# Performance work log

Measured on AMD Instinct MI355X. Metric: run time of the kernel, lower is better.

Reference implementation:

```python
import jax, jax.numpy as jnp
import numpy as np

B, T, I, H, L, C = 64, 512, 128, 512, 3, 5


def setup_inputs() -> dict:
    key = jax.random.key(0)
    ks = jax.random.split(key, 2 + 4 * L + 2)
    s = 1.0 / np.sqrt(H)  # PyTorch RNN init range
    inp = {"x": jax.random.normal(ks[0], (B, T, I), dtype=jnp.float32)}
    in_dims = [I] + [H] * (L - 1)
    for l in range(L):
        k0, k1, k2, k3 = ks[1 + 4 * l:5 + 4 * l]
        inp[f"W_ih{l}"] = jax.random.uniform(k0, (H, in_dims[l]), jnp.float32, -s, s)
        inp[f"W_hh{l}"] = jax.random.uniform(k1, (H, H), jnp.float32, -s, s)
        inp[f"b_ih{l}"] = jax.random.uniform(k2, (H,), jnp.float32, -s, s)
        inp[f"b_hh{l}"] = jax.random.uniform(k3, (H,), jnp.float32, -s, s)
    so = 1.0 / np.sqrt(H)
    inp["W_out"] = jax.random.uniform(ks[-2], (C, H), jnp.float32, -so, so)
    inp["b_out"] = jax.random.uniform(ks[-1], (C,), jnp.float32, -so, so)
    return inp


def _rnn_layer(xs, W_ih, W_hh, b_ih, b_hh):
    # xs: [B, T, D] -> hidden sequence [B, T, H], ReLU RNN recurrence
    h0 = jnp.zeros((xs.shape[0], W_hh.shape[0]), xs.dtype)
    xproj = jnp.einsum('btd,hd->bth', xs, W_ih) + (b_ih + b_hh)  # precompute input GEMM

    def step(h, xp_t):
        h = jax.nn.relu(xp_t + h @ W_hh.T)
        return h, h

    _, ys = jax.lax.scan(step, h0, jnp.swapaxes(xproj, 0, 1))  # scan over time
    return jnp.swapaxes(ys, 0, 1)


def reference(x, W_ih0, W_hh0, b_ih0, b_hh0, W_ih1, W_hh1, b_ih1, b_hh1,
              W_ih2, W_hh2, b_ih2, b_hh2, W_out, b_out):
    h = x
    for W_ih, W_hh, b_ih, b_hh in ((W_ih0, W_hh0, b_ih0, b_hh0),
                                   (W_ih1, W_hh1, b_ih1, b_hh1),
                                   (W_ih2, W_hh2, b_ih2, b_hh2)):
        h = _rnn_layer(h, W_ih, W_hh, b_ih, b_hh)
    # last timestep -> linear head: [B, C]
    return h[:, -1, :] @ W_out.T + b_out
```

## Files before the change

kernel.cpp:

```cpp
#include <hip/hip_runtime.h>

#define BB 64
#define TT 512
#define II 128
#define HH 512
#define CC 5

__global__ __launch_bounds__(256) void gemm_bias_kernel(
    const float* __restrict__ A, const float* __restrict__ W,
    const float* __restrict__ b1, const float* __restrict__ b2,
    float* __restrict__ out, int K)
{
    __shared__ float As[16][132];
    __shared__ float Bs[16][132];
    const int tid = threadIdx.x;
    const int bm = blockIdx.x;
    const int bn = blockIdx.y;
    const int tx = tid & 15;
    const int ty = tid >> 4;
    const int lr = tid >> 2;
    const int lk = (tid & 3) << 2;

    const float* Ab = A + (size_t)bm * 128 * K;
    const float* Wb = W + (size_t)bn * 128 * K;

    float acc[8][8];
#pragma unroll
    for (int i = 0; i < 8; ++i)
#pragma unroll
        for (int j = 0; j < 8; ++j) acc[i][j] = 0.f;

    for (int k0 = 0; k0 < K; k0 += 16) {
        float4 a0 = *(const float4*)(Ab + (size_t)lr * K + k0 + lk);
        float4 a1 = *(const float4*)(Ab + (size_t)(lr + 64) * K + k0 + lk);
        float4 w0 = *(const float4*)(Wb + (size_t)lr * K + k0 + lk);
        float4 w1 = *(const float4*)(Wb + (size_t)(lr + 64) * K + k0 + lk);
        __syncthreads();
        As[lk + 0][lr] = a0.x; As[lk + 1][lr] = a0.y; As[lk + 2][lr] = a0.z; As[lk + 3][lr] = a0.w;
        As[lk + 0][lr + 64] = a1.x; As[lk + 1][lr + 64] = a1.y; As[lk + 2][lr + 64] = a1.z; As[lk + 3][lr + 64] = a1.w;
        Bs[lk + 0][lr] = w0.x; Bs[lk + 1][lr] = w0.y; Bs[lk + 2][lr] = w0.z; Bs[lk + 3][lr] = w0.w;
        Bs[lk + 0][lr + 64] = w1.x; Bs[lk + 1][lr + 64] = w1.y; Bs[lk + 2][lr + 64] = w1.z; Bs[lk + 3][lr + 64] = w1.w;
        __syncthreads();
#pragma unroll
        for (int k = 0; k < 16; ++k) {
            float4 av0 = *(const float4*)&As[k][ty * 8];
            float4 av1 = *(const float4*)&As[k][ty * 8 + 4];
            float4 bv0 = *(const float4*)&Bs[k][tx * 8];
            float4 bv1 = *(const float4*)&Bs[k][tx * 8 + 4];
            float a[8] = {av0.x, av0.y, av0.z, av0.w, av1.x, av1.y, av1.z, av1.w};
            float b[8] = {bv0.x, bv0.y, bv0.z, bv0.w, bv1.x, bv1.y, bv1.z, bv1.w};
#pragma unroll
            for (int i = 0; i < 8; ++i)
#pragma unroll
                for (int j = 0; j < 8; ++j)
                    acc[i][j] = fmaf(a[i], b[j], acc[i][j]);
        }
    }

    const int nb = bn * 128 + tx * 8;
    float bias[8];
#pragma unroll
    for (int j = 0; j < 8; ++j) bias[j] = b1[nb + j] + b2[nb + j];
#pragma unroll
    for (int i = 0; i < 8; ++i) {
        const size_t m = (size_t)bm * 128 + ty * 8 + i;
        float4 o0 = {acc[i][0] + bias[0], acc[i][1] + bias[1], acc[i][2] + bias[2], acc[i][3] + bias[3]};
        float4 o1 = {acc[i][4] + bias[4], acc[i][5] + bias[5], acc[i][6] + bias[6], acc[i][7] + bias[7]};
        *(float4*)(out + m * HH + nb) = o0;
        *(float4*)(out + m * HH + nb + 4) = o1;
    }
}

__global__ __launch_bounds__(512)
__attribute__((amdgpu_waves_per_eu(2, 2)))
void scan_kernel(
    const float* __restrict__ xp, const float* __restrict__ Whh,
    float* __restrict__ y, unsigned long long* hbuf)
{
    __shared__ float hbs[4][2][8 * 68];
    __shared__ int written[8];

    const int tid  = threadIdx.x;
    const int s    = blockIdx.x >> 5;
    const int g    = blockIdx.x & 31;
    const int lane = tid & 63;
    const int wv   = tid >> 6;
    const int rloc = lane >> 3;
    const int kseg = lane & 7;
    const int R    = s * 64 + wv * 8 + rloc;

    const float* wr = Whh + (size_t)R * HH + kseg * 64;
    const float4 w0  = *(const float4*)(wr + 0);
    const float4 w1  = *(const float4*)(wr + 4);
    const float4 w2  = *(const float4*)(wr + 8);
    const float4 w3  = *(const float4*)(wr + 12);
    const float4 w4  = *(const float4*)(wr + 16);
    const float4 w5  = *(const float4*)(wr + 20);
    const float4 w6  = *(const float4*)(wr + 24);
    const float4 w7  = *(const float4*)(wr + 28);
    const float4 w8  = *(const float4*)(wr + 32);
    const float4 w9  = *(const float4*)(wr + 36);
    const float4 w10 = *(const float4*)(wr + 40);
    const float4 w11 = *(const float4*)(wr + 44);
    const float4 w12 = *(const float4*)(wr + 48);
    const float4 w13 = *(const float4*)(wr + 52);
    const float4 w14 = *(const float4*)(wr + 56);
    const float4 w15 = *(const float4*)(wr + 60);

    unsigned long long* gbase = hbuf + (size_t)g * 2048;
    const int gb0 = g * 2, gb1 = g * 2 + 1;

    const int lds_w    = wv * 68 + lane;
    const int self_lds = s * 68 + wv * 8 + rloc;
    const bool pub     = (kseg == 0);
    const bool foreign = (wv != s);

    hbs[0][0][lds_w] = 0.f;
    hbs[0][1][lds_w] = 0.f;
    if (tid < 8) written[tid] = 0;

    float xp0 = 0.f, xp1 = 0.f;
    if (pub) {
        xp0 = xp[(size_t)gb0 * TT * HH + R];
        xp1 = xp[(size_t)gb1 * TT * HH + R];
    }
    __syncthreads();

    for (int t = 0; t < TT; ++t) {
        if (t > 0) {
            for (;;) {
                int m = __hip_atomic_load(&written[0], __ATOMIC_RELAXED,
                                          __HIP_MEMORY_SCOPE_WORKGROUP);
#pragma unroll
                for (int c = 1; c < 8; ++c) {
                    int wc = __hip_atomic_load(&written[c], __ATOMIC_RELAXED,
                                               __HIP_MEMORY_SCOPE_WORKGROUP);
                    m = (wc < m) ? wc : m;
                }
                if (m >= t) break;
            }
            __threadfence_block();
        }

        const int bi = t & 3;
        float a0 = 0.f, a1 = 0.f, c0 = 0.f, c1 = 0.f;
        const float* h0p = &hbs[bi][0][kseg * 68];
        const float* h1p = &hbs[bi][1][kseg * 68];
#define STEP4(WQ, OFF)                                                   \
        {                                                                \
            float4 h0 = *(const float4*)(h0p + (OFF));                   \
            float4 h1 = *(const float4*)(h1p + (OFF));                   \
            a0 = fmaf(WQ.x, h0.x, a0); a1 = fmaf(WQ.y, h0.y, a1);        \
            a0 = fmaf(WQ.z, h0.z, a0); a1 = fmaf(WQ.w, h0.w, a1);        \
            c0 = fmaf(WQ.x, h1.x, c0); c1 = fmaf(WQ.y, h1.y, c1);        \
            c0 = fmaf(WQ.z, h1.z, c0); c1 = fmaf(WQ.w, h1.w, c1);        \
        }
        STEP4(w0, 0)   STEP4(w1, 4)   STEP4(w2, 8)   STEP4(w3, 12)
        STEP4(w4, 16)  STEP4(w5, 20)  STEP4(w6, 24)  STEP4(w7, 28)
        STEP4(w8, 32)  STEP4(w9, 36)  STEP4(w10, 40) STEP4(w11, 44)
        STEP4(w12, 48) STEP4(w13, 52) STEP4(w14, 56) STEP4(w15, 60)
#undef STEP4

        float A = a0 + a1, Bv = c0 + c1;
        A  += __shfl_xor(A, 1);  A  += __shfl_xor(A, 2);  A  += __shfl_xor(A, 4);
        Bv += __shfl_xor(Bv, 1); Bv += __shfl_xor(Bv, 2); Bv += __shfl_xor(Bv, 4);

        const int q = t + 1;
        unsigned long long* slotp = gbase + (q & 3) * 512;
        const unsigned int phase = 1u ^ (((unsigned)(q - 1) >> 2) & 1u);

        float hn0 = 0.f, hn1 = 0.f;
        if (pub) {
            hn0 = fmaxf(A + xp0, 0.f);
            hn1 = fmaxf(Bv + xp1, 0.f);
            if (q < TT) {
                const unsigned long long pkt =
                    (unsigned long long)(__float_as_uint(hn0) | (phase << 31)) |
                    ((unsigned long long)(__float_as_uint(hn1) | (phase << 31)) << 32);
                __hip_atomic_store(slotp + R, pkt,
                                   __ATOMIC_RELAXED, __HIP_MEMORY_SCOPE_AGENT);
                hbs[q & 3][0][self_lds] = hn0;
                hbs[q & 3][1][self_lds] = hn1;
            }
            y[((size_t)gb0 * TT + t) * HH + R] = hn0;
            y[((size_t)gb1 * TT + t) * HH + R] = hn1;
            if (q < TT) {
                xp0 = xp[((size_t)gb0 * TT + q) * HH + R];
                xp1 = xp[((size_t)gb1 * TT + q) * HH + R];
            }
        }

        if (q < TT) {
            if (foreign) {
                unsigned long long u;
                for (;;) {
                    u = __hip_atomic_load(slotp + tid, __ATOMIC_RELAXED,
                                          __HIP_MEMORY_SCOPE_AGENT);
                    if ((((unsigned int)(u >> 31) & 1u) == phase) &&
                        ((unsigned int)(u >> 63) == phase)) break;
                }
                hbs[q & 3][0][lds_w] = __uint_as_float((unsigned int)u & 0x7fffffffu);
                hbs[q & 3][1][lds_w] = __uint_as_float((unsigned int)(u >> 32) & 0x7fffffffu);
            }
            __threadfence_block();
            if (lane == 0)
                __hip_atomic_store(&written[wv], q, __ATOMIC_RELAXED,
                                   __HIP_MEMORY_SCOPE_WORKGROUP);
        }
    }
}

__global__ __launch_bounds__(64) void head_kernel(
    const float* __restrict__ y2, const float* __restrict__ Wout,
    const float* __restrict__ bout, float* __restrict__ out)
{
    const int bc = blockIdx.x;
    const int b = bc / CC, c = bc % CC;
    const int lane = threadIdx.x;
    const float* yrow = y2 + ((size_t)b * TT + (TT - 1)) * HH;
    const float* wrow = Wout + (size_t)c * HH;
    float s = 0.f;
#pragma unroll
    for (int i = 0; i < HH / 64; ++i)
        s = fmaf(yrow[lane + 64 * i], wrow[lane + 64 * i], s);
#pragma unroll
    for (int off = 32; off > 0; off >>= 1) s += __shfl_down(s, off);
    if (lane == 0) out[bc] = s + bout[c];
}

extern "C" void kernel_launch(void* const* d_in, const int* in_sizes, int n_in,
                              void* d_out, int out_size, void* d_ws, size_t ws_size,
                              hipStream_t stream)
{
    const float* x = (const float*)d_in[0];
    const float* W_ih[3] = {(const float*)d_in[1], (const float*)d_in[5], (const float*)d_in[9]};
    const float* W_hh[3] = {(const float*)d_in[2], (const float*)d_in[6], (const float*)d_in[10]};
    const float* b_ih[3] = {(const float*)d_in[3], (const float*)d_in[7], (const float*)d_in[11]};
    const float* b_hh[3] = {(const float*)d_in[4], (const float*)d_in[8], (const float*)d_in[12]};
    const float* W_out = (const float*)d_in[13];
    const float* b_out = (const float*)d_in[14];
    float* out = (float*)d_out;

    float* ws   = (float*)d_ws;
    float* Y    = ws;
    float* XP   = ws + (size_t)BB * TT * HH;
    unsigned long long* hbuf = (unsigned long long*)(XP + (size_t)BB * TT * HH);

    const size_t hbuf_bytes = 32 * 4 * 512 * sizeof(unsigned long long);
    const dim3 ggrid(256, 4, 1);

    gemm_bias_kernel<<<ggrid, 256, 0, stream>>>(x, W_ih[0], b_ih[0], b_hh[0], XP, II);
    (void)hipMemsetAsync(hbuf, 0, hbuf_bytes, stream);
    scan_kernel<<<256, 512, 0, stream>>>(XP, W_hh[0], Y, hbuf);
    gemm_bias_kernel<<<ggrid, 256, 0, stream>>>(Y, W_ih[1], b_ih[1], b_hh[1], XP, HH);
    (void)hipMemsetAsync(hbuf, 0, hbuf_bytes, stream);
    scan_kernel<<<256, 512, 0, stream>>>(XP, W_hh[1], Y, hbuf);
    gemm_bias_kernel<<<ggrid, 256, 0, stream>>>(Y, W_ih[2], b_ih[2], b_hh[2], XP, HH);
    (void)hipMemsetAsync(hbuf, 0, hbuf_bytes, stream);
    scan_kernel<<<256, 512, 0, stream>>>(XP, W_hh[2], Y, hbuf);
    head_kernel<<<BB * CC, 64, 0, stream>>>(Y, W_out, b_out, out);
}
```

Baseline: 2.673 ms.

## Pipeline layer 0 and layer 1 scans concurrently with fused input projection

Replaces the per-layer GEMM + scan sequence with a wavefront pipeline. Layer-0 scan blocks and fused layer-1 blocks run in one launch. Layer 1 consumes layer-0 outputs per timestep through flagged global packets and computes the input projection inline alongside the recurrence, and layer 2 runs as a separate fused kernel. This removes two GEMM launches and the serialization between layer scans. In exchange it adds large memsets of full-history flag buffers, more global polling traffic, and relies on all 512 co-resident blocks making forward progress.

New measurement: 4.267 ms. 1.6x slower.

```diff
diff --git a/kernel.cpp b/kernel.cpp
--- a/kernel.cpp
+++ b/kernel.cpp
@@ -5,6 +5,43 @@
 #define II 128
 #define HH 512
 #define CC 5
+
+
+#define FPAD(v) ((((v) >> 5) * 36) + ((v) & 31))
+#define M31LO(u) __uint_as_float((unsigned int)(u) & 0x7fffffffu)
+#define M31HI(u) __uint_as_float((unsigned int)((u) >> 32) & 0x7fffffffu)
+
+struct FSh {
+    float hbs[2][4][16 * 36];
+    float ybs[2][4][16 * 36];
+    int written[8];
+};
+struct SSh {
+    float hbs[4][2][8 * 68];
+    int written[8];
+};
+union ShU { FSh f; SSh s; };
+
+__device__ __forceinline__ bool prdy(unsigned long long u, int set) {
+    const unsigned int hi = (unsigned int)(u >> 63) & 1u;
+    const unsigned int lo = (unsigned int)(u >> 31) & 1u;
+    return set ? (hi && lo) : (hi && !lo);
+}
+
+template <int M>
+__device__ __forceinline__ const unsigned long long* src_addr(
+    const unsigned long long* mainb, const unsigned long long* sideb,
+    int gp, int t, int v, int half)
+{
+    if constexpr (M == 2) {
+        return mainb + (((size_t)(2 * gp + half) * 512 + t) * 512 + v);
+    } else if constexpr (M == 0) {
+        if (t >= 2) return mainb + (((size_t)(2 * gp + half) * 512 + (t - 2)) * 512 + v);
+        return sideb + (((size_t)(gp * 2 + t) * 512 + v) * 2 + half);
+    } else {
+        return mainb + (((size_t)gp * 512 + t) * 512 + v) * 2 + half;
+    }
+}
 
 __global__ __launch_bounds__(256) void gemm_bias_kernel(
     const float* __restrict__ A, const float* __restrict__ W,
@@ -71,18 +108,12 @@
     }
 }
 
-__global__ __launch_bounds__(512)
-__attribute__((amdgpu_waves_per_eu(2, 2)))
-void scan_kernel(
-    const float* __restrict__ xp, const float* __restrict__ Whh,
-    float* __restrict__ y, unsigned long long* hbuf)
-{
-    __shared__ float hbs[4][2][8 * 68];
-    __shared__ int written[8];
-
+__device__ void scan0_body(ShU* sh, int g, int s,
+                           const float* __restrict__ xp,
+                           const float* __restrict__ Whh,
+                           unsigned long long* __restrict__ ybuf0)
+{
     const int tid  = threadIdx.x;
-    const int s    = blockIdx.x >> 5;
-    const int g    = blockIdx.x & 31;
     const int lane = tid & 63;
     const int wv   = tid >> 6;
     const int rloc = lane >> 3;
@@ -107,7 +138,7 @@
     const float4 w14 = *(const float4*)(wr + 56);
     const float4 w15 = *(const float4*)(wr + 60);
 
-    unsigned long long* gbase = hbuf + (size_t)g * 2048;
+    unsigned long long* gb = ybuf0 + (size_t)g * (512 * 512);
     const int gb0 = g * 2, gb1 = g * 2 + 1;
 
     const int lds_w    = wv * 68 + lane;
@@ -115,9 +146,9 @@
     const bool pub     = (kseg == 0);
     const bool foreign = (wv != s);
 
-    hbs[0][0][lds_w] = 0.f;
-    hbs[0][1][lds_w] = 0.f;
-    if (tid < 8) written[tid] = 0;
+    sh->s.hbs[0][0][lds_w] = 0.f;
+    sh->s.hbs[0][1][lds_w] = 0.f;
+    if (tid < 8) sh->s.written[tid] = 0;
 
     float xp0 = 0.f, xp1 = 0.f;
     if (pub) {
@@ -129,11 +160,11 @@
     for (int t = 0; t < TT; ++t) {
         if (t > 0) {
             for (;;) {
-                int m = __hip_atomic_load(&written[0], __ATOMIC_RELAXED,
+                int m = __hip_atomic_load(&sh->s.written[0], __ATOMIC_RELAXED,
                                           __HIP_MEMORY_SCOPE_WORKGROUP);
 #pragma unroll
                 for (int c = 1; c < 8; ++c) {
-                    int wc = __hip_atomic_load(&written[c], __ATOMIC_RELAXED,
+                    int wc = __hip_atomic_load(&sh->s.written[c], __ATOMIC_RELAXED,
                                                __HIP_MEMORY_SCOPE_WORKGROUP);
                     m = (wc < m) ? wc : m;
                 }
@@ -144,8 +175,8 @@
 
         const int bi = t & 3;
         float a0 = 0.f, a1 = 0.f, c0 = 0.f, c1 = 0.f;
-        const float* h0p = &hbs[bi][0][kseg * 68];
-        const float* h1p = &hbs[bi][1][kseg * 68];
+        const float* h0p = &sh->s.hbs[bi][0][kseg * 68];
+        const float* h1p = &sh->s.hbs[bi][1][kseg * 68];
 #define STEP4(WQ, OFF)                                                   \
         {                                                                \
             float4 h0 = *(const float4*)(h0p + (OFF));                   \
@@ -153,7 +184,7 @@
             a0 = fmaf(WQ.x, h0.x, a0); a1 = fmaf(WQ.y, h0.y, a1);        \
             a0 = fmaf(WQ.z, h0.z, a0); a1 = fmaf(WQ.w, h0.w, a1);        \
             c0 = fmaf(WQ.x, h1.x, c0); c1 = fmaf(WQ.y, h1.y, c1);        \
-            c0 = fmaf(WQ.z, h1.z, c0); c1 = fmaf(WQ.w, h1.w, c1);        \
+            c0 = fmaf(WQ.z, h1.z, c0); c1 = fmaf(WQ.w, h1.w, c1);       \
         }
         STEP4(w0, 0)   STEP4(w1, 4)   STEP4(w2, 8)   STEP4(w3, 12)
         STEP4(w4, 16)  STEP4(w5, 20)  STEP4(w6, 24)  STEP4(w7, 28)
@@ -166,25 +197,17 @@
         Bv += __shfl_xor(Bv, 1); Bv += __shfl_xor(Bv, 2); Bv += __shfl_xor(Bv, 4);
 
         const int q = t + 1;
-        unsigned long long* slotp = gbase + (q & 3) * 512;
-        const unsigned int phase = 1u ^ (((unsigned)(q - 1) >> 2) & 1u);
-
-        float hn0 = 0.f, hn1 = 0.f;
         if (pub) {
-            hn0 = fmaxf(A + xp0, 0.f);
-            hn1 = fmaxf(Bv + xp1, 0.f);
+            const float hn0 = fmaxf(A + xp0, 0.f);
+            const float hn1 = fmaxf(Bv + xp1, 0.f);
+            const unsigned long long pkt =
+                (unsigned long long)(__float_as_uint(hn0) | 0x80000000u) |
+                ((unsigned long long)(__float_as_uint(hn1) | 0x80000000u) << 32);
+            __hip_atomic_store(gb + (size_t)t * 512 + R, pkt,
+                               __ATOMIC_RELAXED, __HIP_MEMORY_SCOPE_AGENT);
             if (q < TT) {
-                const unsigned long long pkt =
-                    (unsigned long long)(__float_as_uint(hn0) | (phase << 31)) |
-                    ((unsigned long long)(__float_as_uint(hn1) | (phase << 31)) << 32);
-                __hip_atomic_store(slotp + R, pkt,
-                                   __ATOMIC_RELAXED, __HIP_MEMORY_SCOPE_AGENT);
-                hbs[q & 3][0][self_lds] = hn0;
-                hbs[q & 3][1][self_lds] = hn1;
-            }
-            y[((size_t)gb0 * TT + t) * HH + R] = hn0;
-            y[((size_t)gb1 * TT + t) * HH + R] = hn1;
-            if (q < TT) {
+                sh->s.hbs[q & 3][0][self_lds] = hn0;
+                sh->s.hbs[q & 3][1][self_lds] = hn1;
                 xp0 = xp[((size_t)gb0 * TT + q) * HH + R];
                 xp1 = xp[((size_t)gb1 * TT + q) * HH + R];
             }
@@ -192,37 +215,239 @@
 
         if (q < TT) {
             if (foreign) {
+                const unsigned long long* pp = gb + (size_t)t * 512 + tid;
                 unsigned long long u;
                 for (;;) {
-                    u = __hip_atomic_load(slotp + tid, __ATOMIC_RELAXED,
-                                          __HIP_MEMORY_SCOPE_AGENT);
-                    if ((((unsigned int)(u >> 31) & 1u) == phase) &&
-                        ((unsigned int)(u >> 63) == phase)) break;
-                }
-                hbs[q & 3][0][lds_w] = __uint_as_float((unsigned int)u & 0x7fffffffu);
-                hbs[q & 3][1][lds_w] = __uint_as_float((unsigned int)(u >> 32) & 0x7fffffffu);
+                    u = __hip_atomic_load(pp, __ATOMIC_RELAXED, __HIP_MEMORY_SCOPE_AGENT);
+                    if (prdy(u, 1)) break;
+                }
+                sh->s.hbs[q & 3][0][lds_w] = M31LO(u);
+                sh->s.hbs[q & 3][1][lds_w] = M31HI(u);
             }
             __threadfence_block();
             if (lane == 0)
-                __hip_atomic_store(&written[wv], q, __ATOMIC_RELAXED,
+                __hip_atomic_store(&sh->s.written[wv], q, __ATOMIC_RELAXED,
                                    __HIP_MEMORY_SCOPE_WORKGROUP);
         }
     }
 }
 
+template <int YAM, int YSET, int HAM>
+__device__ void fused_body(ShU* sh, const int gp, const int s,
+                           const float* __restrict__ Whh,
+                           const float* __restrict__ Wih,
+                           const float* __restrict__ bih,
+                           const float* __restrict__ bhh,
+                           const unsigned long long* __restrict__ ysrc,
+                           const unsigned long long* __restrict__ yside,
+                           unsigned long long* __restrict__ hmain,
+                           unsigned long long* __restrict__ hside)
+{
+    const int tid  = threadIdx.x;
+    const int lane = tid & 63;
+    const int wv   = tid >> 6;
+    const int kseg = lane & 15;
+    const int rloc = lane >> 4;
+    const int R    = s * 32 + wv * 4 + rloc;
+    const bool pub = (kseg == 0);
+
+    const float* whp = Whh + (size_t)R * HH + kseg * 32;
+    const float* wip = Wih + (size_t)R * HH + kseg * 32;
+    float4 wh[8], wi[8];
+#pragma unroll
+    for (int i = 0; i < 8; ++i) {
+        wh[i] = *(const float4*)(whp + 4 * i);
+        wi[i] = *(const float4*)(wip + 4 * i);
+    }
+    const float bias = bih[R] + bhh[R];
+
+    const int c      = 2 * wv + (lane >> 5);
+    const bool hduty = (c != s);
+    const int hv     = c * 32 + (lane & 31);
+    const int v0     = tid;
+
+#pragma unroll
+    for (int b = 0; b < 4; ++b) sh->f.hbs[0][b][FPAD(v0)] = 0.f;
+    {
+        const unsigned long long* a0 = src_addr<YAM>(ysrc, yside, gp, 0, v0, 0);
+        const unsigned long long* a1 = src_addr<YAM>(ysrc, yside, gp, 0, v0, 1);
+        bool d0 = false, d1 = false;
+        for (;;) {
+            unsigned long long u0 = 0, u1 = 0;
+            if (!d0) u0 = __hip_atomic_load(a0, __ATOMIC_RELAXED, __HIP_MEMORY_SCOPE_AGENT);
+            if (!d1) u1 = __hip_atomic_load(a1, __ATOMIC_RELAXED, __HIP_MEMORY_SCOPE_AGENT);
+            if (!d0 && prdy(u0, YSET)) {
+                sh->f.ybs[0][0][FPAD(v0)] = M31LO(u0);
+                sh->f.ybs[0][1][FPAD(v0)] = M31HI(u0);
+                d0 = true;
+            }
+            if (!d1 && prdy(u1, YSET)) {
+                sh->f.ybs[0][2][FPAD(v0)] = M31LO(u1);
+                sh->f.ybs[0][3][FPAD(v0)] = M31HI(u1);
+                d1 = true;
+            }
+            if (d0 && d1) break;
+        }
+    }
+    if (tid < 8) sh->f.written[tid] = 0;
+    __syncthreads();
+
+    for (int t = 0; t < TT; ++t) {
+        const int bi = t & 1;
+        if (t > 0) {
+            for (;;) {
+                int m = __hip_atomic_load(&sh->f.written[0], __ATOMIC_RELAXED,
+                                          __HIP_MEMORY_SCOPE_WORKGROUP);
+#pragma unroll
+                for (int k = 1; k < 8; ++k) {
+                    int wk = __hip_atomic_load(&sh->f.written[k], __ATOMIC_RELAXED,
+                                               __HIP_MEMORY_SCOPE_WORKGROUP);
+                    m = (wk < m) ? wk : m;
+                }
+                if (m >= t) break;
+            }
+            __threadfence_block();
+        }
+
+        float s0[4] = {0.f, 0.f, 0.f, 0.f}, s1[4] = {0.f, 0.f, 0.f, 0.f};
+        const float* hb = &sh->f.hbs[bi][0][kseg * 36];
+        const float* yb = &sh->f.ybs[bi][0][kseg * 36];
+#pragma unroll
+        for (int i = 0; i < 8; ++i) {
+            const float4 wh4 = wh[i], wi4 = wi[i];
+#pragma unroll
+            for (int b = 0; b < 4; ++b) {
+                const float4 h4 = *(const float4*)(hb + b * 576 + 4 * i);
+                const float4 y4 = *(const float4*)(yb + b * 576 + 4 * i);
+                s0[b] = fmaf(wh4.x, h4.x, s0[b]); s1[b] = fmaf(wh4.y, h4.y, s1[b]);
+                s0[b] = fmaf(wh4.z, h4.z, s0[b]); s1[b] = fmaf(wh4.w, h4.w, s1[b]);
+                s0[b] = fmaf(wi4.x, y4.x, s0[b]); s1[b] = fmaf(wi4.y, y4.y, s1[b]);
+                s0[b] = fmaf(wi4.z, y4.z, s0[b]); s1[b] = fmaf(wi4.w, y4.w, s1[b]);
+            }
+        }
+        float A[4];
+#pragma unroll
+        for (int b = 0; b < 4; ++b) {
+            A[b] = s0[b] + s1[b];
+            A[b] += __shfl_xor(A[b], 1);
+            A[b] += __shfl_xor(A[b], 2);
+            A[b] += __shfl_xor(A[b], 4);
+            A[b] += __shfl_xor(A[b], 8);
+        }
+
+        const int q = t + 1;
+        if (pub) {
+            float hn[4];
+#pragma unroll
+            for (int b = 0; b < 4; ++b) hn[b] = fmaxf(A[b] + bias, 0.f);
+#pragma unroll
+            for (int half = 0; half < 2; ++half) {
+                const unsigned int lo = __float_as_uint(hn[half * 2]);
+                const unsigned int hi = __float_as_uint(hn[half * 2 + 1]) | 0x80000000u;
+                const unsigned long long pkt =
+                    (unsigned long long)lo | ((unsigned long long)hi << 32);
+                unsigned long long* dst =
+                    (unsigned long long*)src_addr<HAM>(hmain, hside, gp, t, R, half);
+                __hip_atomic_store(dst, pkt, __ATOMIC_RELAXED, __HIP_MEMORY_SCOPE_AGENT);
+            }
+            if (q < TT) {
+#pragma unroll
+                for (int b = 0; b < 4; ++b) sh->f.hbs[q & 1][b][FPAD(R)] = hn[b];
+            }
+        }
+
+        if (q < TT) {
+            const int qb = q & 1;
+            const unsigned long long* py0 = src_addr<YAM>(ysrc, yside, gp, q, v0, 0);
+            const unsigned long long* py1 = src_addr<YAM>(ysrc, yside, gp, q, v0, 1);
+            const unsigned long long* ph0 = src_addr<HAM>(hmain, hside, gp, t, hv, 0);
+            const unsigned long long* ph1 = src_addr<HAM>(hmain, hside, gp, t, hv, 1);
+            bool dy0 = false, dy1 = false, dh0 = !hduty, dh1 = !hduty;
+            for (;;) {
+                unsigned long long u0 = 0, u1 = 0, u2 = 0, u3 = 0;
+                if (!dy0) u0 = __hip_atomic_load(py0, __ATOMIC_RELAXED, __HIP_MEMORY_SCOPE_AGENT);
+                if (!dy1) u1 = __hip_atomic_load(py1, __ATOMIC_RELAXED, __HIP_MEMORY_SCOPE_AGENT);
+                if (!dh0) u2 = __hip_atomic_load(ph0, __ATOMIC_RELAXED, __HIP_MEMORY_SCOPE_AGENT);
+                if (!dh1) u3 = __hip_atomic_load(ph1, __ATOMIC_RELAXED, __HIP_MEMORY_SCOPE_AGENT);
+                if (!dy0 && prdy(u0, YSET)) {
+                    sh->f.ybs[qb][0][FPAD(v0)] = M31LO(u0);
+                    sh->f.ybs[qb][1][FPAD(v0)] = M31HI(u0);
+                    dy0 = true;
+                }
+                if (!dy1 && prdy(u1, YSET)) {
+                    sh->f.ybs[qb][2][FPAD(v0)] = M31LO(u1);
+                    sh->f.ybs[qb][3][FPAD(v0)] = M31HI(u1);
+                    dy1 = true;
+                }
+                if (!dh0 && prdy(u2, 0)) {
+                    sh->f.hbs[qb][0][FPAD(hv)] = M31LO(u2);
+                    sh->f.hbs[qb][1][FPAD(hv)] = M31HI(u2);
+                    dh0 = true;
+                }
+                if (!dh1 && prdy(u3, 0)) {
+                    sh->f.hbs[qb][2][FPAD(hv)] = M31LO(u3);
+                    sh->f.hbs[qb][3][FPAD(hv)] = M31HI(u3);
+                    dh1 = true;
+                }
+                if (dy0 && dy1 && dh0 && dh1) break;
+            }
+            __threadfence_block();
+            if (lane == 0)
+                __hip_atomic_store(&sh->f.written[wv], q, __ATOMIC_RELAXED,
+                                   __HIP_MEMORY_SCOPE_WORKGROUP);
+        }
+    }
+}
+
+__global__ __launch_bounds__(512, 4) void pipeA_kernel(
+    const float* __restrict__ xp0, const float* __restrict__ Whh0,
+    unsigned long long* __restrict__ RA,
+    const float* __restrict__ Whh1, const float* __restrict__ Wih1,
+    const float* __restrict__ bih1, const float* __restrict__ bhh1,
+    unsigned long long* __restrict__ SIDE)
+{
+    __shared__ ShU sh;
+    const int bi = blockIdx.x;
+    if (bi < 256) {
+        fused_body<2, 1, 0>(&sh, bi & 15, bi >> 4, Whh1, Wih1, bih1, bhh1,
+                            RA, SIDE, RA, SIDE);
+    } else {
+        const int j = bi - 256;
+        scan0_body(&sh, j & 31, j >> 5, xp0, Whh0, RA);
+    }
+}
+
+__global__ __launch_bounds__(512, 2) void layer2_kernel(
+    const unsigned long long* __restrict__ RA,
+    const unsigned long long* __restrict__ SIDE,
+    const float* __restrict__ Whh2, const float* __restrict__ Wih2,
+    const float* __restrict__ bih2, const float* __restrict__ bhh2,
+    unsigned long long* __restrict__ RB)
+{
+    __shared__ ShU sh;
+    const int bi = blockIdx.x;
+    fused_body<0, 0, 1>(&sh, bi & 15, bi >> 4, Whh2, Wih2, bih2, bhh2,
+                        RA, SIDE, RB, RB);
+}
+
 __global__ __launch_bounds__(64) void head_kernel(
-    const float* __restrict__ y2, const float* __restrict__ Wout,
+    const unsigned long long* __restrict__ y2, const float* __restrict__ Wout,
     const float* __restrict__ bout, float* __restrict__ out)
 {
     const int bc = blockIdx.x;
     const int b = bc / CC, c = bc % CC;
     const int lane = threadIdx.x;
-    const float* yrow = y2 + ((size_t)b * TT + (TT - 1)) * HH;
+    const int gp = b >> 2, j = b & 3, half = j >> 1, odd = j & 1;
+    const unsigned int* ybase =
+        (const unsigned int*)(y2 + ((size_t)(gp * 512 + (TT - 1)) * 512) * 2);
     const float* wrow = Wout + (size_t)c * HH;
     float s = 0.f;
 #pragma unroll
-    for (int i = 0; i < HH / 64; ++i)
-        s = fmaf(yrow[lane + 64 * i], wrow[lane + 64 * i], s);
+    for (int i = 0; i < HH / 64; ++i) {
+        const int h = lane + 64 * i;
+        const float v = __uint_as_float(ybase[(size_t)h * 4 + half * 2 + odd] & 0x7fffffffu);
+        s = fmaf(v, wrow[h], s);
+    }
 #pragma unroll
     for (int off = 32; off > 0; off >>= 1) s += __shfl_down(s, off);
     if (lane == 0) out[bc] = s + bout[c];
@@ -232,6 +457,7 @@
                               void* d_out, int out_size, void* d_ws, size_t ws_size,
                               hipStream_t stream)
 {
+    (void)in_sizes; (void)n_in; (void)out_size; (void)ws_size;
     const float* x = (const float*)d_in[0];
     const float* W_ih[3] = {(const float*)d_in[1], (const float*)d_in[5], (const float*)d_in[9]};
     const float* W_hh[3] = {(const float*)d_in[2], (const float*)d_in[6], (const float*)d_in[10]};
@@ -241,22 +467,22 @@
     const float* b_out = (const float*)d_in[14];
     float* out = (float*)d_out;
 
-    float* ws   = (float*)d_ws;
-    float* Y    = ws;
-    float* XP   = ws + (size_t)BB * TT * HH;
-    unsigned long long* hbuf = (unsigned long long*)(XP + (size_t)BB * TT * HH);
-
-    const size_t hbuf_bytes = 32 * 4 * 512 * sizeof(unsigned long long);
-    const dim3 ggrid(256, 4, 1);
-
-    gemm_bias_kernel<<<ggrid, 256, 0, stream>>>(x, W_ih[0], b_ih[0], b_hh[0], XP, II);
-    (void)hipMemsetAsync(hbuf, 0, hbuf_bytes, stream);
-    scan_kernel<<<256, 512, 0, stream>>>(XP, W_hh[0], Y, hbuf);
-    gemm_bias_kernel<<<ggrid, 256, 0, stream>>>(Y, W_ih[1], b_ih[1], b_hh[1], XP, HH);
-    (void)hipMemsetAsync(hbuf, 0, hbuf_bytes, stream);
-    scan_kernel<<<256, 512, 0, stream>>>(XP, W_hh[1], Y, hbuf);
-    gemm_bias_kernel<<<ggrid, 256, 0, stream>>>(Y, W_ih[2], b_ih[2], b_hh[2], XP, HH);
-    (void)hipMemsetAsync(hbuf, 0, hbuf_bytes, stream);
-    scan_kernel<<<256, 512, 0, stream>>>(XP, W_hh[2], Y, hbuf);
-    head_kernel<<<BB * CC, 64, 0, stream>>>(Y, W_out, b_out, out);
-}
+    unsigned long long* RA  = (unsigned long long*)d_ws;
+    float*              XP  = (float*)((char*)d_ws + ((size_t)64 << 20));
+    unsigned long long* RB  = (unsigned long long*)XP;
+    unsigned long long* SIDE = (unsigned long long*)((char*)d_ws + ((size_t)128 << 20));
+
+    (void)hipMemsetAsync(RA, 0, (size_t)64 << 20, stream);
+    (void)hipMemsetAsync(SIDE, 0xFF, (size_t)32768 * 8, stream);
+
+    gemm_bias_kernel<<<dim3(256, 4, 1), 256, 0, stream>>>(x, W_ih[0], b_ih[0], b_hh[0], XP, II);
+
+    pipeA_kernel<<<512, 512, 0, stream>>>(XP, W_hh[0], RA,
+                                          W_hh[1], W_ih[1], b_ih[1], b_hh[1], SIDE);
+
+    (void)hipMemsetAsync(RB, 0, (size_t)64 << 20, stream);
+
+    layer2_kernel<<<256, 512, 0, stream>>>(RA, SIDE, W_hh[2], W_ih[2], b_ih[2], b_hh[2], RB);
+
+    head_kernel<<<BB * CC, 64, 0, stream>>>(RB, W_out, b_out, out);
+}
```

## Split recurrent matvec by K-slice per wave and reduce partials in publisher wave

Applied to the files above, without the earlier changes.

The scan kernel is reorganised so each wave holds a 64-column K-slice of its block's 64 W_hh rows, instead of 8 full rows. Each wave now needs only its own slice of the previous hidden state, which it polls from global memory, so waves no longer wait on a block-wide all-waves-ready flag before computing. Per-wave partial sums are reduced with DPP adds, written to a double-buffered shared array and summed by the single publisher wave. That wave applies bias and ReLU, then publishes the new hidden values. This shortens the per-timestep dependency chain, but it adds an extra shared-memory round trip and concentrates the reduction wait on one wave.

Measured after the change: 2.817 ms. +5.4%, slower.

```diff
diff --git a/kernel.cpp b/kernel.cpp
--- a/kernel.cpp
+++ b/kernel.cpp
@@ -71,141 +71,161 @@
     }
 }
 
+template <int CTRL>
+__device__ __forceinline__ float dpp_add(float v) {
+    const int t = __builtin_amdgcn_update_dpp(0, __float_as_int(v), CTRL, 0xf, 0xf, true);
+    return v + __int_as_float(t);
+}
+__device__ __forceinline__ float reduce8(float v) {
+    v = dpp_add<0xB1>(v);
+    v = dpp_add<0x4E>(v);
+    v = dpp_add<0x141>(v);
+    return v;
+}
+
 __global__ __launch_bounds__(512)
 __attribute__((amdgpu_waves_per_eu(2, 2)))
 void scan_kernel(
     const float* __restrict__ xp, const float* __restrict__ Whh,
     float* __restrict__ y, unsigned long long* hbuf)
 {
-    __shared__ float hbs[4][2][8 * 68];
-    __shared__ int written[8];
+    __shared__ float lh[4][2][512];
+    __shared__ float P[2][8][64][2];
+    __shared__ int pflag[8];
 
     const int tid  = threadIdx.x;
     const int s    = blockIdx.x >> 5;
     const int g    = blockIdx.x & 31;
     const int lane = tid & 63;
     const int wv   = tid >> 6;
-    const int rloc = lane >> 3;
-    const int kseg = lane & 7;
-    const int R    = s * 64 + wv * 8 + rloc;
-
-    const float* wr = Whh + (size_t)R * HH + kseg * 64;
-    const float4 w0  = *(const float4*)(wr + 0);
-    const float4 w1  = *(const float4*)(wr + 4);
-    const float4 w2  = *(const float4*)(wr + 8);
-    const float4 w3  = *(const float4*)(wr + 12);
-    const float4 w4  = *(const float4*)(wr + 16);
-    const float4 w5  = *(const float4*)(wr + 20);
-    const float4 w6  = *(const float4*)(wr + 24);
-    const float4 w7  = *(const float4*)(wr + 28);
-    const float4 w8  = *(const float4*)(wr + 32);
-    const float4 w9  = *(const float4*)(wr + 36);
-    const float4 w10 = *(const float4*)(wr + 40);
-    const float4 w11 = *(const float4*)(wr + 44);
-    const float4 w12 = *(const float4*)(wr + 48);
-    const float4 w13 = *(const float4*)(wr + 52);
-    const float4 w14 = *(const float4*)(wr + 56);
-    const float4 w15 = *(const float4*)(wr + 60);
+    const int rgrp = lane >> 3;
+    const int khi  = lane & 7;
+    const int ks   = wv * 8 + khi;
+
+    const float* wb = Whh + (size_t)(s * 64 + rgrp * 8) * HH + ks * 8;
+    float4 W0[8], W1[8];
+#pragma unroll
+    for (int j = 0; j < 8; ++j) {
+        W0[j] = *(const float4*)(wb + (size_t)j * HH);
+        W1[j] = *(const float4*)(wb + (size_t)j * HH + 4);
+    }
 
     unsigned long long* gbase = hbuf + (size_t)g * 2048;
     const int gb0 = g * 2, gb1 = g * 2 + 1;
-
-    const int lds_w    = wv * 68 + lane;
-    const int self_lds = s * 68 + wv * 8 + rloc;
-    const bool pub     = (kseg == 0);
-    const bool foreign = (wv != s);
-
-    hbs[0][0][lds_w] = 0.f;
-    hbs[0][1][lds_w] = 0.f;
-    if (tid < 8) written[tid] = 0;
-
-    float xp0 = 0.f, xp1 = 0.f;
-    if (pub) {
-        xp0 = xp[(size_t)gb0 * TT * HH + R];
-        xp1 = xp[(size_t)gb1 * TT * HH + R];
+    const bool ispub = (wv == s);
+    const int prow = s * 64 + lane;
+
+    lh[0][0][tid] = 0.f;
+    lh[0][1][tid] = 0.f;
+    if (tid < 8) pflag[tid] = 0;
+
+    float xq0 = 0.f, xq1 = 0.f;
+    if (ispub) {
+        xq0 = xp[(size_t)gb0 * TT * HH + prow];
+        xq1 = xp[(size_t)gb1 * TT * HH + prow];
     }
     __syncthreads();
 
     for (int t = 0; t < TT; ++t) {
-        if (t > 0) {
+        const int bi = t & 3;
+        const int par = t & 1;
+        const int q = t + 1;
+
+        const float* h0p = &lh[bi][0][wv * 64 + khi * 8];
+        const float* h1p = &lh[bi][1][wv * 64 + khi * 8];
+        const float4 ha0 = *(const float4*)(h0p);
+        const float4 ha1 = *(const float4*)(h0p + 4);
+        const float4 hb0 = *(const float4*)(h1p);
+        const float4 hb1 = *(const float4*)(h1p + 4);
+
+        float pa[8], pb[8];
+#pragma unroll
+        for (int j = 0; j < 8; ++j) {
+            float u = W0[j].x * ha0.x;
+            u = fmaf(W0[j].y, ha0.y, u); u = fmaf(W0[j].z, ha0.z, u); u = fmaf(W0[j].w, ha0.w, u);
+            u = fmaf(W1[j].x, ha1.x, u); u = fmaf(W1[j].y, ha1.y, u);
+            u = fmaf(W1[j].z, ha1.z, u); u = fmaf(W1[j].w, ha1.w, u);
+            pa[j] = u;
+            float v = W0[j].x * hb0.x;
+            v = fmaf(W0[j].y, hb0.y, v); v = fmaf(W0[j].z, hb0.z, v); v = fmaf(W0[j].w, hb0.w, v);
+            v = fmaf(W1[j].x, hb1.x, v); v = fmaf(W1[j].y, hb1.y, v);
+            v = fmaf(W1[j].z, hb1.z, v); v = fmaf(W1[j].w, hb1.w, v);
+            pb[j] = v;
+        }
+
+#pragma unroll
+        for (int j = 0; j < 8; ++j) {
+            pa[j] = reduce8(pa[j]);
+            pb[j] = reduce8(pb[j]);
+        }
+
+        if (khi == 0) {
+            float* pw = &P[par][wv][rgrp * 8][0];
+            float4 o0 = {pa[0], pb[0], pa[1], pb[1]};
+            float4 o1 = {pa[2], pb[2], pa[3], pb[3]};
+            float4 o2 = {pa[4], pb[4], pa[5], pb[5]};
+            float4 o3 = {pa[6], pb[6], pa[7], pb[7]};
+            *(float4*)(pw + 0)  = o0;
+            *(float4*)(pw + 4)  = o1;
+            *(float4*)(pw + 8)  = o2;
+            *(float4*)(pw + 12) = o3;
+        }
+        __threadfence_block();
+        if (lane == 0)
+            __hip_atomic_store(&pflag[wv], q, __ATOMIC_RELAXED,
+                               __HIP_MEMORY_SCOPE_WORKGROUP);
+
+        if (ispub) {
             for (;;) {
-                int m = __hip_atomic_load(&written[0], __ATOMIC_RELAXED,
+                int m = __hip_atomic_load(&pflag[0], __ATOMIC_RELAXED,
                                           __HIP_MEMORY_SCOPE_WORKGROUP);
 #pragma unroll
                 for (int c = 1; c < 8; ++c) {
-                    int wc = __hip_atomic_load(&written[c], __ATOMIC_RELAXED,
+                    int wc = __hip_atomic_load(&pflag[c], __ATOMIC_RELAXED,
                                                __HIP_MEMORY_SCOPE_WORKGROUP);
                     m = (wc < m) ? wc : m;
                 }
-                if (m >= t) break;
+                if (m >= q) break;
             }
             __threadfence_block();
-        }
-
-        const int bi = t & 3;
-        float a0 = 0.f, a1 = 0.f, c0 = 0.f, c1 = 0.f;
-        const float* h0p = &hbs[bi][0][kseg * 68];
-        const float* h1p = &hbs[bi][1][kseg * 68];
-#define STEP4(WQ, OFF)                                                   \
-        {                                                                \
-            float4 h0 = *(const float4*)(h0p + (OFF));                   \
-            float4 h1 = *(const float4*)(h1p + (OFF));                   \
-            a0 = fmaf(WQ.x, h0.x, a0); a1 = fmaf(WQ.y, h0.y, a1);        \
-            a0 = fmaf(WQ.z, h0.z, a0); a1 = fmaf(WQ.w, h0.w, a1);        \
-            c0 = fmaf(WQ.x, h1.x, c0); c1 = fmaf(WQ.y, h1.y, c1);        \
-            c0 = fmaf(WQ.z, h1.z, c0); c1 = fmaf(WQ.w, h1.w, c1);        \
-        }
-        STEP4(w0, 0)   STEP4(w1, 4)   STEP4(w2, 8)   STEP4(w3, 12)
-        STEP4(w4, 16)  STEP4(w5, 20)  STEP4(w6, 24)  STEP4(w7, 28)
-        STEP4(w8, 32)  STEP4(w9, 36)  STEP4(w10, 40) STEP4(w11, 44)
-        STEP4(w12, 48) STEP4(w13, 52) STEP4(w14, 56) STEP4(w15, 60)
-#undef STEP4
-
-        float A = a0 + a1, Bv = c0 + c1;
-        A  += __shfl_xor(A, 1);  A  += __shfl_xor(A, 2);  A  += __shfl_xor(A, 4);
-        Bv += __shfl_xor(Bv, 1); Bv += __shfl_xor(Bv, 2); Bv += __shfl_xor(Bv, 4);
-
-        const int q = t + 1;
-        unsigned long long* slotp = gbase + (q & 3) * 512;
-        const unsigned int phase = 1u ^ (((unsigned)(q - 1) >> 2) & 1u);
-
-        float hn0 = 0.f, hn1 = 0.f;
-        if (pub) {
-            hn0 = fmaxf(A + xp0, 0.f);
-            hn1 = fmaxf(Bv + xp1, 0.f);
+
+            float s0 = xq0, s1 = xq1;
+#pragma unroll
+            for (int w = 0; w < 8; ++w) {
+                const float2 pr = *(const float2*)&P[par][w][lane][0];
+                s0 += pr.x;
+                s1 += pr.y;
+            }
+            const float hn0 = fmaxf(s0, 0.f);
+            const float hn1 = fmaxf(s1, 0.f);
+
             if (q < TT) {
+                unsigned long long* slotp = gbase + (q & 3) * 512;
+                const unsigned int phase = 1u ^ (((unsigned)(q - 1) >> 2) & 1u);
                 const unsigned long long pkt =
                     (unsigned long long)(__float_as_uint(hn0) | (phase << 31)) |
                     ((unsigned long long)(__float_as_uint(hn1) | (phase << 31)) << 32);
-                __hip_atomic_store(slotp + R, pkt,
+                __hip_atomic_store(slotp + prow, pkt,
                                    __ATOMIC_RELAXED, __HIP_MEMORY_SCOPE_AGENT);
-                hbs[q & 3][0][self_lds] = hn0;
-                hbs[q & 3][1][self_lds] = hn1;
-            }
-            y[((size_t)gb0 * TT + t) * HH + R] = hn0;
-            y[((size_t)gb1 * TT + t) * HH + R] = hn1;
-            if (q < TT) {
-                xp0 = xp[((size_t)gb0 * TT + q) * HH + R];
-                xp1 = xp[((size_t)gb1 * TT + q) * HH + R];
-            }
-        }
-
-        if (q < TT) {
-            if (foreign) {
-                unsigned long long u;
-                for (;;) {
-                    u = __hip_atomic_load(slotp + tid, __ATOMIC_RELAXED,
-                                          __HIP_MEMORY_SCOPE_AGENT);
-                    if ((((unsigned int)(u >> 31) & 1u) == phase) &&
-                        ((unsigned int)(u >> 63) == phase)) break;
-                }
-                hbs[q & 3][0][lds_w] = __uint_as_float((unsigned int)u & 0x7fffffffu);
-                hbs[q & 3][1][lds_w] = __uint_as_float((unsigned int)(u >> 32) & 0x7fffffffu);
-            }
-            __threadfence_block();
-            if (lane == 0)
-                __hip_atomic_store(&written[wv], q, __ATOMIC_RELAXED,
-                                   __HIP_MEMORY_SCOPE_WORKGROUP);
+                lh[q & 3][0][prow] = hn0;
+                lh[q & 3][1][prow] = hn1;
+                xq0 = xp[((size_t)gb0 * TT + q) * HH + prow];
+                xq1 = xp[((size_t)gb1 * TT + q) * HH + prow];
+            }
+            y[((size_t)gb0 * TT + t) * HH + prow] = hn0;
+            y[((size_t)gb1 * TT + t) * HH + prow] = hn1;
+        } else if (q < TT) {
+            const unsigned long long* pp = gbase + (q & 3) * 512 + tid;
+            const unsigned int phase = 1u ^ (((unsigned)(q - 1) >> 2) & 1u);
+            unsigned long long u;
+            for (;;) {
+                u = __hip_atomic_load(pp, __ATOMIC_RELAXED,
+                                      __HIP_MEMORY_SCOPE_AGENT);
+                if ((((unsigned int)(u >> 31) & 1u) == phase) &&
+                    ((unsigned int)(u >> 63) == phase)) break;
+            }
+            lh[q & 3][0][tid] = __uint_as_float((unsigned int)u & 0x7fffffffu);
+            lh[q & 3][1][tid] = __uint_as_float((unsigned int)(u >> 32) & 0x7fffffffu);
         }
     }
 }
@@ -232,6 +252,7 @@
                               void* d_out, int out_size, void* d_ws, size_t ws_size,
                               hipStream_t stream)
 {
+    (void)in_sizes; (void)n_in; (void)out_size; (void)ws_size;
     const float* x = (const float*)d_in[0];
     const float* W_ih[3] = {(const float*)d_in[1], (const float*)d_in[5], (const float*)d_in[9]};
     const float* W_hh[3] = {(const float*)d_in[2], (const float*)d_in[6], (const float*)d_in[10]};
```
